# Kernel optimization log

Hardware: AMD Instinct MI355X
Metric: run time of the kernel (lower is better)

Reference implementation:

```python
import jax, jax.numpy as jnp
import numpy as np

N, C, SI, VI, H, R = 10000, 2, 128, 16, 4, 32
SH, VH = SI // H, VI // H  # 32, 4
EPS = 1e-8

def _vnorm(x, axis):
    # clamped L2 norm, matches _norm_no_nan
    return jnp.sqrt(jnp.clip(jnp.sum(x * x, axis=axis), EPS, None))

def _gvp_full(s, v, wh, ws_w, ws_b, wv, wsv_w, wsv_b):
    # GVP with activations=(silu, sigmoid), vector_gate=True, vi=vo
    vh = jnp.swapaxes(v, -1, -2) @ wh            # [..., 3, h]
    vn = _vnorm(vh, -2)                          # [..., h]
    so = jnp.concatenate([s, vn], -1) @ ws_w + ws_b
    vo = jnp.swapaxes(vh @ wv, -1, -2)           # [..., vo, 3]
    gate = jax.nn.sigmoid(jax.nn.sigmoid(so) @ wsv_w + wsv_b)
    return jax.nn.silu(so), vo * gate[..., None]

def setup_inputs():
    key = jax.random.key(0)
    ks = iter(jax.random.split(key, 40))
    def lin(i, o):
        return jax.random.normal(next(ks), (i, o), jnp.float32) / np.sqrt(i)
    def bias(o):
        return 0.02 * jax.random.normal(next(ks), (o,), jnp.float32)
    inp = {}
    inp['s'] = jax.random.normal(next(ks), (N, C, SI), jnp.float32)
    inp['v'] = jax.random.normal(next(ks), (N, C, VI, 3), jnp.float32)
    # weight_proj: GVP((SI,VI)->(R,0)), no activations; h_dim = max(VI,0) = VI
    inp['wp_wh'] = lin(VI, VI); inp['wp_ws_w'] = lin(VI + SI, R); inp['wp_ws_b'] = bias(R)
    # to_q/k/v: GVP((SI,VI)->(SI,VI)), silu/sigmoid, vector_gate; h_dim = VI
    for p in ('q', 'k', 'vv'):
        inp[p + '_wh'] = lin(VI, VI)
        inp[p + '_ws_w'] = lin(VI + SI, SI); inp[p + '_ws_b'] = bias(SI)
        inp[p + '_wv'] = lin(VI, VI)
        inp[p + '_wsv_w'] = lin(SI, VI); inp[p + '_wsv_b'] = bias(VI)
    # attn_gvp_long: GVP((2*SH, 2*VH) -> (1,0)), no activations; h_dim = 2*VH
    inp['attn_wh'] = lin(2 * VH, 2 * VH)
    inp['attn_ws_w'] = lin(2 * VH + 2 * SH, 1); inp['attn_ws_b'] = bias(1)
    return inp

def reference(s, v, wp_wh, wp_ws_w, wp_ws_b,
              q_wh, q_ws_w, q_ws_b, q_wv, q_wsv_w, q_wsv_b,
              k_wh, k_ws_w, k_ws_b, k_wv, k_wsv_w, k_wsv_b,
              vv_wh, vv_ws_w, vv_ws_b, vv_wv, vv_wsv_w, vv_wsv_b,
              attn_wh, attn_ws_w, attn_ws_b):
    n, c = s.shape[:2]
    # ---- Compress: softmax-pool N -> R anchors ----
    vh = jnp.swapaxes(v, -1, -2) @ wp_wh          # [N,C,3,VI]
    vn = _vnorm(vh, -2)                            # [N,C,VI]
    pw = jnp.concatenate([s, vn], -1) @ wp_ws_w + wp_ws_b  # [N,C,R]
    pw = jax.nn.softmax(pw, axis=0)                # softmax over nodes
    s_g = jnp.einsum('nca,ncs->acs', pw, s)        # [R,C,SI] (includes transpose(0,1))
    v_g = jnp.einsum('nca,ncvd->acvd', pw, v)      # [R,C,VI,3]
    # ---- q from nodes, k/v from anchors ----
    qs, qv = _gvp_full(s, v, q_wh, q_ws_w, q_ws_b, q_wv, q_wsv_w, q_wsv_b)
    ks, kv = _gvp_full(s_g, v_g, k_wh, k_ws_w, k_ws_b, k_wv, k_wsv_w, k_wsv_b)
    vs, vv_ = _gvp_full(s_g, v_g, vv_wh, vv_ws_w, vv_ws_b, vv_wv, vv_wsv_w, vv_wsv_b)
    qs = qs.reshape(n, c, H, SH); qv = qv.reshape(n, c, H, VH, 3)
    ks = ks.reshape(R, c, H, SH); kv = kv.reshape(R, c, H, VH, 3)
    vs = vs.reshape(R, c, H, SH); vv_ = vv_.reshape(R, c, H, VH, 3)
    # ---- attention GVP on cat(q, k): split weights instead of materializing concat ----
    wh_q, wh_k = attn_wh[:VH], attn_wh[VH:]        # wh @ cat(qv,kv) = qv@wh_q + kv@wh_k
    qh = jnp.swapaxes(qv, -1, -2) @ wh_q           # [N,C,H,3,2VH]
    kh = jnp.swapaxes(kv, -1, -2) @ wh_k           # [R,C,H,3,2VH]
    vn2 = _vnorm(qh[:, None] + kh[None], -2)       # [N,R,C,H,2VH]
    ws_q = attn_ws_w[:SH]; ws_k = attn_ws_w[SH:2 * SH]; ws_n = attn_ws_w[2 * SH:]
    e = (qs @ ws_q)[:, None] + (ks @ ws_k)[None] + vn2 @ ws_n + attn_ws_b  # [N,R,C,H,1]
    e = e[..., 0] / np.sqrt(SH)
    alpha = jax.nn.softmax(e, axis=1)              # softmax over anchors (dim=1)
    # ---- Broadcast: weighted sum of anchor values ----
    out_s = jnp.einsum('nrch,rchd->nchd', alpha, vs).reshape(n, c, SI)
    out_v = jnp.einsum('nrch,rchde->nchde', alpha, vv_).reshape(n, c, VI, 3)
    return out_s, out_v
```

## Files before the change

kernel.cpp:

```cpp
#include <hip/hip_runtime.h>
#include <hip/hip_bf16.h>


#define N_  10000
#define C_  2
#define SI_ 128
#define VI_ 16
#define H_  4
#define R_  32
#define SH_ 32
#define VH_ 4
#define NC_ (N_*C_)

typedef const float* __restrict__ fptr;

__device__ __forceinline__ float sigm(float x){ return 1.f/(1.f+__expf(-x)); }

#define OFF_LG  0
#define OFF_EQH 640000
#define OFF_SG  2720000
#define OFF_ST  2731264
#define OFF_TKH 2731392
#define OFF_TEK 2737536
#define OFF_TVS 2737792
#define OFF_TVV 2745984

__global__ __launch_bounds__(256) void kA(
    fptr s, fptr v,
    fptr wp_wh, fptr wp_ws_w, fptr wp_ws_b,
    fptr q_wh, fptr q_ws_w, fptr q_ws_b, fptr q_wv, fptr q_wsv_w, fptr q_wsv_b,
    fptr attn_wh, fptr attn_ws_w,
    float* __restrict__ lg, float* __restrict__ eqh)
{
  __shared__ __align__(16) float XT[160*20];
  __shared__ __align__(16) float VVs[16*48];
  __shared__ __align__(16) float VHQ[16*48];
  __shared__ __align__(16) float SO[16*128];
  __shared__ __align__(16) float GATE[16*16];
  __shared__ __align__(16) float QV[16*48];

  const int tid  = threadIdx.x;
  const int row0 = blockIdx.x * 16;

  for (int idx = tid; idx < 16*128; idx += 256){
    int r = idx >> 7, j = idx & 127;
    XT[j*20 + r] = s[(row0+r)*128 + j];
  }
  for (int idx = tid; idx < 16*48; idx += 256){
    int r = idx / 48, k = idx - r*48;
    VVs[r*48 + k] = v[(row0+r)*48 + k];
  }
  __syncthreads();

  for (int t = tid; t < 512; t += 256){
    int r = t >> 5, ii = t & 31, path = ii >> 4, i = ii & 15;
    fptr wh = path ? wp_wh : q_wh;
    float h0=0.f, h1=0.f, h2=0.f;
    #pragma unroll
    for (int j = 0; j < 16; j++){
      float w = wh[j*16 + i];
      h0 = fmaf(VVs[r*48 + j*3 + 0], w, h0);
      h1 = fmaf(VVs[r*48 + j*3 + 1], w, h1);
      h2 = fmaf(VVs[r*48 + j*3 + 2], w, h2);
    }
    float vn = sqrtf(fmaxf(h0*h0 + h1*h1 + h2*h2, 1e-8f));
    if (!path){
      VHQ[r*48 +  0 + i] = h0;
      VHQ[r*48 + 16 + i] = h1;
      VHQ[r*48 + 32 + i] = h2;
      XT[(128+i)*20 + r] = vn;
    } else {
      XT[(144+i)*20 + r] = vn;
    }
  }
  __syncthreads();

  {
    const int col = tid & 127, rg = tid >> 7;
    float bqs = q_ws_b[col];
    float acc[8];
    #pragma unroll
    for (int k = 0; k < 8; k++) acc[k] = bqs;
    #pragma unroll 4
    for (int j = 0; j < 144; j++){
      float w = q_ws_w[j*128 + col];
      const float* xp = &XT[j*20 + rg*8];
      float4 x0 = *(const float4*)xp;
      float4 x1 = *(const float4*)(xp + 4);
      acc[0] = fmaf(x0.x, w, acc[0]); acc[1] = fmaf(x0.y, w, acc[1]);
      acc[2] = fmaf(x0.z, w, acc[2]); acc[3] = fmaf(x0.w, w, acc[3]);
      acc[4] = fmaf(x1.x, w, acc[4]); acc[5] = fmaf(x1.y, w, acc[5]);
      acc[6] = fmaf(x1.z, w, acc[6]); acc[7] = fmaf(x1.w, w, acc[7]);
    }
    #pragma unroll
    for (int k = 0; k < 8; k++) SO[(rg*8 + k)*128 + col] = acc[k];
  }
  {
    const int col = tid & 31, rg = tid >> 5;
    float bp = wp_ws_b[col];
    float a0 = bp, a1 = bp;
    #pragma unroll 4
    for (int j = 0; j < 144; j++){
      int jj = (j < 128) ? j : (j + 16);
      float w = wp_ws_w[j*32 + col];
      const float* xp = &XT[jj*20 + rg*2];
      a0 = fmaf(xp[0], w, a0);
      a1 = fmaf(xp[1], w, a1);
    }
    lg[(row0 + rg*2 + 0)*32 + col] = a0;
    lg[(row0 + rg*2 + 1)*32 + col] = a1;
  }
  __syncthreads();

  {
    const int r = tid >> 4, g = tid & 15;
    float ga = q_wsv_b[g];
    for (int o = 0; o < 128; o++)
      ga = fmaf(sigm(SO[r*128 + o]), q_wsv_w[o*16 + g], ga);
    GATE[r*16 + g] = sigm(ga);
  }
  if (tid < 64){
    const int r = tid >> 2, h = tid & 3;
    float e = 0.f;
    #pragma unroll
    for (int t = 0; t < 32; t++){
      float so = SO[r*128 + h*32 + t];
      e = fmaf(so * sigm(so), attn_ws_w[t], e);
    }
    eqh[(row0 + r)*104 + h] = e;
  }
  __syncthreads();

  for (int t = tid; t < 16*48; t += 256){
    int r = t / 48, k = t - r*48, i = k / 3, d = k - i*3;
    float acc = 0.f;
    #pragma unroll
    for (int j = 0; j < 16; j++)
      acc = fmaf(VHQ[r*48 + d*16 + j], q_wv[j*16 + i], acc);
    QV[r*48 + k] = acc * GATE[r*16 + i];
  }
  __syncthreads();

  for (int t = tid; t < 16*96; t += 256){
    int r = t / 96, k = t - r*96;
    int h = k / 24, rem = k - h*24, d = rem >> 3, ee = rem & 7;
    float acc = 0.f;
    #pragma unroll
    for (int i = 0; i < 4; i++)
      acc = fmaf(QV[r*48 + (h*4 + i)*3 + d], attn_wh[i*8 + ee], acc);
    eqh[(row0 + r)*104 + 8 + k] = acc;
  }
}

__global__ __launch_bounds__(256) void kStats(const float* __restrict__ lg,
                                              float* __restrict__ st)
{
  const int q = blockIdx.x;
  const int c = q >> 5, a = q & 31;
  const int tid = threadIdx.x;
  __shared__ float red[256];

  float m = -1e30f;
  for (int n = tid; n < N_; n += 256)
    m = fmaxf(m, lg[(n*2 + c)*32 + a]);
  red[tid] = m; __syncthreads();
  for (int s2 = 128; s2 > 0; s2 >>= 1){
    if (tid < s2) red[tid] = fmaxf(red[tid], red[tid + s2]);
    __syncthreads();
  }
  const float mx = red[0];
  __syncthreads();

  float sm = 0.f;
  for (int n = tid; n < N_; n += 256)
    sm += __expf(lg[(n*2 + c)*32 + a] - mx);
  red[tid] = sm; __syncthreads();
  for (int s2 = 128; s2 > 0; s2 >>= 1){
    if (tid < s2) red[tid] += red[tid + s2];
    __syncthreads();
  }
  if (tid == 0){ st[q*2] = mx; st[q*2 + 1] = red[0]; }
}

#define CHUNK_ 50
__global__ __launch_bounds__(256) void kAccum(const float* __restrict__ lg,
                                              const float* __restrict__ st,
                                              fptr s, fptr v,
                                              float* __restrict__ sg)
{
  const int b = blockIdx.x, c = b & 1, chunk = b >> 1;
  const int n0 = chunk * CHUNK_;
  const int tid = threadIdx.x;
  const int ag = tid >> 5, dl = tid & 31;

  float mx[4], dn[4];
  #pragma unroll
  for (int aa = 0; aa < 4; aa++){
    int a = ag*4 + aa;
    mx[aa] = st[(c*32 + a)*2];
    dn[aa] = 1.f / st[(c*32 + a)*2 + 1];
  }
  float acc[4][6] = {};
  for (int n = n0; n < n0 + CHUNK_; n++){
    const int rc = n*2 + c;
    float pw[4];
    #pragma unroll
    for (int aa = 0; aa < 4; aa++)
      pw[aa] = __expf(lg[rc*32 + ag*4 + aa] - mx[aa]) * dn[aa];
    #pragma unroll
    for (int dd = 0; dd < 6; dd++){
      int d = dl + 32*dd;
      if (d < 176){
        float xv = (d < 128) ? s[rc*128 + d] : v[rc*48 + d - 128];
        #pragma unroll
        for (int aa = 0; aa < 4; aa++)
          acc[aa][dd] = fmaf(pw[aa], xv, acc[aa][dd]);
      }
    }
  }
  #pragma unroll
  for (int aa = 0; aa < 4; aa++)
    #pragma unroll
    for (int dd = 0; dd < 6; dd++){
      int d = dl + 32*dd;
      if (d < 176)
        atomicAdd(&sg[(c*32 + ag*4 + aa)*176 + d], acc[aa][dd]);
    }
}

__global__ __launch_bounds__(256) void kSmall(
    const float* __restrict__ sg,
    fptr k_wh, fptr k_ws_w, fptr k_ws_b, fptr k_wv, fptr k_wsv_w, fptr k_wsv_b,
    fptr vv_wh, fptr vv_ws_w, fptr vv_ws_b, fptr vv_wv, fptr vv_wsv_w, fptr vv_wsv_b,
    fptr attn_wh, fptr attn_ws_w,
    float* __restrict__ tkh, float* __restrict__ tek,
    float* __restrict__ tvs, float* __restrict__ tvv)
{
  const int b = blockIdx.x, r = b >> 1, c = b & 1;
  const int tid = threadIdx.x;
  __shared__ float X[176];
  __shared__ float VN[2][16];
  __shared__ float VH[2][48];
  __shared__ float SOk[128], SOv[128];
  __shared__ float G[2][16];
  __shared__ float KV[48];

  if (tid < 176) X[tid] = sg[(c*32 + r)*176 + tid];
  __syncthreads();

  if (tid < 32){
    int path = tid >> 4, i = tid & 15;
    fptr wh = path ? vv_wh : k_wh;
    float h0=0.f, h1=0.f, h2=0.f;
    #pragma unroll
    for (int j = 0; j < 16; j++){
      float w = wh[j*16 + i];
      h0 = fmaf(X[128 + j*3 + 0], w, h0);
      h1 = fmaf(X[128 + j*3 + 1], w, h1);
      h2 = fmaf(X[128 + j*3 + 2], w, h2);
    }
    VH[path][ 0 + i] = h0; VH[path][16 + i] = h1; VH[path][32 + i] = h2;
    VN[path][i] = sqrtf(fmaxf(h0*h0 + h1*h1 + h2*h2, 1e-8f));
  }
  __syncthreads();

  {
    int path = tid >> 7, col = tid & 127;
    fptr W  = path ? vv_ws_w : k_ws_w;
    fptr Bb = path ? vv_ws_b : k_ws_b;
    float so = Bb[col];
    for (int j = 0; j < 128; j++) so = fmaf(X[j], W[j*128 + col], so);
    #pragma unroll
    for (int i = 0; i < 16; i++)  so = fmaf(VN[path][i], W[(128+i)*128 + col], so);
    (path ? SOv : SOk)[col] = so;
  }
  __syncthreads();

  if (tid < 32){
    int path = tid >> 4, g = tid & 15;
    fptr Wsv = path ? vv_wsv_w : k_wsv_w;
    fptr Bsv = path ? vv_wsv_b : k_wsv_b;
    const float* SOp = path ? SOv : SOk;
    float ga = Bsv[g];
    for (int o = 0; o < 128; o++)
      ga = fmaf(sigm(SOp[o]), Wsv[o*16 + g], ga);
    G[path][g] = sigm(ga);
  } else if (tid < 36){
    int h = tid - 32;
    float e = 0.f;
    #pragma unroll
    for (int t = 0; t < 32; t++){
      float so = SOk[h*32 + t];
      e = fmaf(so * sigm(so), attn_ws_w[32 + t], e);
    }
    tek[(r*2 + c)*4 + h] = e;
  } else if (tid >= 64 && tid < 192){
    int o = tid - 64;
    float so = SOv[o];
    tvs[(r*2 + c)*128 + o] = so * sigm(so);
  }
  __syncthreads();

  if (tid < 96){
    int path = tid / 48, k = tid % 48, i = k / 3, d = k - i*3;
    fptr Wv = path ? vv_wv : k_wv;
    float vo = 0.f;
    #pragma unroll
    for (int j = 0; j < 16; j++)
      vo = fmaf(VH[path][d*16 + j], Wv[j*16 + i], vo);
    float gv = vo * G[path][i];
    if (path == 0) KV[k] = gv;
    else {
      int h = i >> 2, ii = i & 3;
      tvv[(((r*2 + c)*4 + h)*4 + ii)*3 + d] = gv;
    }
  }
  __syncthreads();

  if (tid < 96){
    int h = tid / 24, rem = tid % 24, d = rem >> 3, ee = rem & 7;
    float acc = 0.f;
    #pragma unroll
    for (int i = 0; i < 4; i++)
      acc = fmaf(KV[(h*4 + i)*3 + d], attn_wh[(4 + i)*8 + ee], acc);
    tkh[((r*2 + c)*4 + h)*24 + d*8 + ee] = acc;
  }
}

__global__ __launch_bounds__(256, 2) void kAttn(
    const float* __restrict__ eqh,
    const float* __restrict__ tkh, const float* __restrict__ tek,
    const float* __restrict__ tvs, const float* __restrict__ tvv,
    fptr attn_ws_w, fptr attn_ws_b,
    float* __restrict__ out)
{
  __shared__ __align__(16) float KH[6144];
  __shared__ __align__(16) float EK[256];
  __shared__ __align__(16) float VS[256*36];
  __shared__ __align__(16) float VVt[3072];
  const int tid = threadIdx.x;

  for (int i = tid; i < 6144; i += 256) KH[i] = tkh[i];
  if (tid < 256) EK[tid] = tek[tid];
  for (int i = tid; i < 8192; i += 256){ int base = i >> 5, t = i & 31; VS[base*36 + t] = tvs[i]; }
  for (int i = tid; i < 3072; i += 256) VVt[i] = tvv[i];

  float wsn[8];
  #pragma unroll
  for (int ee = 0; ee < 8; ee++) wsn[ee] = attn_ws_w[64 + ee];
  const float wb = attn_ws_b[0];
  __syncthreads();

  const int row = blockIdx.x*64 + (tid >> 2);
  const int h = tid & 3;
  if (row < NC_){
    const int c = row & 1;
    const float eq = eqh[row*104 + h];
    float qh[24];
    const float4* qp = (const float4*)&eqh[row*104 + 8 + h*24];
    #pragma unroll
    for (int k = 0; k < 6; k++){
      float4 t4 = qp[k];
      qh[k*4+0] = t4.x; qh[k*4+1] = t4.y; qh[k*4+2] = t4.z; qh[k*4+3] = t4.w;
    }
    float e[32];
    float em = -1e30f;
    #pragma unroll
    for (int r = 0; r < 32; r++){
      const int base = (r*2 + c)*4 + h;
      const float* khp = &KH[base*24];
      float en = 0.f;
      #pragma unroll
      for (int ee = 0; ee < 8; ee++){
        float a0 = qh[ee]      + khp[ee];
        float a1 = qh[8 + ee]  + khp[8 + ee];
        float a2 = qh[16 + ee] + khp[16 + ee];
        en = fmaf(sqrtf(fmaxf(a0*a0 + a1*a1 + a2*a2, 1e-8f)), wsn[ee], en);
      }
      float ev = (eq + EK[base] + en + wb) * 0.17677669529663687f;
      e[r] = ev; em = fmaxf(em, ev);
    }
    float den = 0.f;
    #pragma unroll
    for (int r = 0; r < 32; r++){ e[r] = __expf(e[r] - em); den += e[r]; }
    const float inv = 1.f / den;
    float accs[32] = {};
    float accv[12] = {};
    #pragma unroll
    for (int r = 0; r < 32; r++){
      const int base = (r*2 + c)*4 + h;
      const float al = e[r] * inv;
      const float* vsp = &VS[base*36];
      #pragma unroll
      for (int t = 0; t < 32; t++) accs[t] = fmaf(al, vsp[t], accs[t]);
      const float* vvp = &VVt[base*12];
      #pragma unroll
      for (int k = 0; k < 12; k++) accv[k] = fmaf(al, vvp[k], accv[k]);
    }
    float* po = &out[row*128 + h*32];
    #pragma unroll
    for (int t = 0; t < 32; t++) po[t] = accs[t];
    float* pv = &out[NC_*128 + row*48 + h*12];
    #pragma unroll
    for (int k = 0; k < 12; k++) pv[k] = accv[k];
  }
}

extern "C" void kernel_launch(void* const* d_in, const int* in_sizes, int n_in,
                              void* d_out, int out_size, void* d_ws, size_t ws_size,
                              hipStream_t stream)
{
  fptr s        = (fptr)d_in[0];
  fptr v        = (fptr)d_in[1];
  fptr wp_wh    = (fptr)d_in[2];
  fptr wp_ws_w  = (fptr)d_in[3];
  fptr wp_ws_b  = (fptr)d_in[4];
  fptr q_wh     = (fptr)d_in[5];
  fptr q_ws_w   = (fptr)d_in[6];
  fptr q_ws_b   = (fptr)d_in[7];
  fptr q_wv     = (fptr)d_in[8];
  fptr q_wsv_w  = (fptr)d_in[9];
  fptr q_wsv_b  = (fptr)d_in[10];
  fptr k_wh     = (fptr)d_in[11];
  fptr k_ws_w   = (fptr)d_in[12];
  fptr k_ws_b   = (fptr)d_in[13];
  fptr k_wv     = (fptr)d_in[14];
  fptr k_wsv_w  = (fptr)d_in[15];
  fptr k_wsv_b  = (fptr)d_in[16];
  fptr vv_wh    = (fptr)d_in[17];
  fptr vv_ws_w  = (fptr)d_in[18];
  fptr vv_ws_b  = (fptr)d_in[19];
  fptr vv_wv    = (fptr)d_in[20];
  fptr vv_wsv_w = (fptr)d_in[21];
  fptr vv_wsv_b = (fptr)d_in[22];
  fptr attn_wh  = (fptr)d_in[23];
  fptr attn_ws_w= (fptr)d_in[24];
  fptr attn_ws_b= (fptr)d_in[25];

  float* ws  = (float*)d_ws;
  float* lg  = ws + OFF_LG;
  float* eqh = ws + OFF_EQH;
  float* sg  = ws + OFF_SG;
  float* st  = ws + OFF_ST;
  float* tkh = ws + OFF_TKH;
  float* tek = ws + OFF_TEK;
  float* tvs = ws + OFF_TVS;
  float* tvv = ws + OFF_TVV;

  hipMemsetAsync(sg, 0, 11264*sizeof(float), stream);

  kA<<<NC_/16, 256, 0, stream>>>(s, v, wp_wh, wp_ws_w, wp_ws_b,
                                 q_wh, q_ws_w, q_ws_b, q_wv, q_wsv_w, q_wsv_b,
                                 attn_wh, attn_ws_w, lg, eqh);
  kStats<<<64, 256, 0, stream>>>(lg, st);
  kAccum<<<2*(N_/CHUNK_), 256, 0, stream>>>(lg, st, s, v, sg);
  kSmall<<<64, 256, 0, stream>>>(sg,
                                 k_wh, k_ws_w, k_ws_b, k_wv, k_wsv_w, k_wsv_b,
                                 vv_wh, vv_ws_w, vv_ws_b, vv_wv, vv_wsv_w, vv_wsv_b,
                                 attn_wh, attn_ws_w, tkh, tek, tvs, tvv);
  kAttn<<<(NC_ + 63)/64, 256, 0, stream>>>(eqh, tkh, tek, tvs, tvv,
                                           attn_ws_w, attn_ws_b, (float*)d_out);
}
```

Measured before the change: 272.0 us.

## Transpose logits layout, precompute sigmoid once, and widen attention blocks

```diff
diff --git a/kernel.cpp b/kernel.cpp
--- a/kernel.cpp
+++ b/kernel.cpp
@@ -32,12 +32,14 @@
     fptr attn_wh, fptr attn_ws_w,
     float* __restrict__ lg, float* __restrict__ eqh)
 {
-  __shared__ __align__(16) float XT[160*20];
+  __shared__ __align__(16) float ARENA[160*20];
   __shared__ __align__(16) float VVs[16*48];
   __shared__ __align__(16) float VHQ[16*48];
   __shared__ __align__(16) float SO[16*128];
   __shared__ __align__(16) float GATE[16*16];
   __shared__ __align__(16) float QV[16*48];
+  float* const XT  = ARENA;
+  float* const SIG = ARENA;
 
   const int tid  = threadIdx.x;
   const int row0 = blockIdx.x * 16;
@@ -75,16 +77,16 @@
   }
   __syncthreads();
 
+  const int colA = tid & 127, rgA = tid >> 7;
+  float acc[8];
   {
-    const int col = tid & 127, rg = tid >> 7;
-    float bqs = q_ws_b[col];
-    float acc[8];
+    float bqs = q_ws_b[colA];
     #pragma unroll
     for (int k = 0; k < 8; k++) acc[k] = bqs;
     #pragma unroll 4
     for (int j = 0; j < 144; j++){
-      float w = q_ws_w[j*128 + col];
-      const float* xp = &XT[j*20 + rg*8];
+      float w = q_ws_w[j*128 + colA];
+      const float* xp = &XT[j*20 + rgA*8];
       float4 x0 = *(const float4*)xp;
       float4 x1 = *(const float4*)(xp + 4);
       acc[0] = fmaf(x0.x, w, acc[0]); acc[1] = fmaf(x0.y, w, acc[1]);
@@ -92,8 +94,6 @@
       acc[4] = fmaf(x1.x, w, acc[4]); acc[5] = fmaf(x1.y, w, acc[5]);
       acc[6] = fmaf(x1.z, w, acc[6]); acc[7] = fmaf(x1.w, w, acc[7]);
     }
-    #pragma unroll
-    for (int k = 0; k < 8; k++) SO[(rg*8 + k)*128 + col] = acc[k];
   }
   {
     const int col = tid & 31, rg = tid >> 5;
@@ -107,48 +107,62 @@
       a0 = fmaf(xp[0], w, a0);
       a1 = fmaf(xp[1], w, a1);
     }
-    lg[(row0 + rg*2 + 0)*32 + col] = a0;
-    lg[(row0 + rg*2 + 1)*32 + col] = a1;
+    const int n = (row0 >> 1) + rg;
+    lg[(     col)*N_ + n] = a0;
+    lg[(32 + col)*N_ + n] = a1;
+  }
+  __syncthreads();
+
+  #pragma unroll
+  for (int k = 0; k < 8; k++){
+    float so = acc[k];
+    float sg_ = sigm(so);
+    SIG[(rgA*8 + k)*128 + colA] = sg_;
+    SO [(rgA*8 + k)*128 + colA] = so * sg_;
   }
   __syncthreads();
 
   {
     const int r = tid >> 4, g = tid & 15;
     float ga = q_wsv_b[g];
-    for (int o = 0; o < 128; o++)
-      ga = fmaf(sigm(SO[r*128 + o]), q_wsv_w[o*16 + g], ga);
+    #pragma unroll 8
+    for (int o = 0; o < 128; o += 4){
+      float4 s4 = *(const float4*)&SIG[r*128 + o];
+      ga = fmaf(s4.x, q_wsv_w[(o+0)*16 + g], ga);
+      ga = fmaf(s4.y, q_wsv_w[(o+1)*16 + g], ga);
+      ga = fmaf(s4.z, q_wsv_w[(o+2)*16 + g], ga);
+      ga = fmaf(s4.w, q_wsv_w[(o+3)*16 + g], ga);
+    }
     GATE[r*16 + g] = sigm(ga);
   }
   if (tid < 64){
     const int r = tid >> 2, h = tid & 3;
     float e = 0.f;
     #pragma unroll
-    for (int t = 0; t < 32; t++){
-      float so = SO[r*128 + h*32 + t];
-      e = fmaf(so * sigm(so), attn_ws_w[t], e);
-    }
+    for (int t = 0; t < 32; t++)
+      e = fmaf(SO[r*128 + h*32 + t], attn_ws_w[t], e);
     eqh[(row0 + r)*104 + h] = e;
   }
   __syncthreads();
 
   for (int t = tid; t < 16*48; t += 256){
     int r = t / 48, k = t - r*48, i = k / 3, d = k - i*3;
-    float acc = 0.f;
+    float a = 0.f;
     #pragma unroll
     for (int j = 0; j < 16; j++)
-      acc = fmaf(VHQ[r*48 + d*16 + j], q_wv[j*16 + i], acc);
-    QV[r*48 + k] = acc * GATE[r*16 + i];
+      a = fmaf(VHQ[r*48 + d*16 + j], q_wv[j*16 + i], a);
+    QV[r*48 + k] = a * GATE[r*16 + i];
   }
   __syncthreads();
 
   for (int t = tid; t < 16*96; t += 256){
     int r = t / 96, k = t - r*96;
     int h = k / 24, rem = k - h*24, d = rem >> 3, ee = rem & 7;
-    float acc = 0.f;
+    float a = 0.f;
     #pragma unroll
     for (int i = 0; i < 4; i++)
-      acc = fmaf(QV[r*48 + (h*4 + i)*3 + d], attn_wh[i*8 + ee], acc);
-    eqh[(row0 + r)*104 + 8 + k] = acc;
+      a = fmaf(QV[r*48 + (h*4 + i)*3 + d], attn_wh[i*8 + ee], a);
+    eqh[(row0 + r)*104 + 8 + k] = a;
   }
 }
 
@@ -156,13 +170,12 @@
                                               float* __restrict__ st)
 {
   const int q = blockIdx.x;
-  const int c = q >> 5, a = q & 31;
   const int tid = threadIdx.x;
+  const float* col = lg + q*N_;
   __shared__ float red[256];
 
   float m = -1e30f;
-  for (int n = tid; n < N_; n += 256)
-    m = fmaxf(m, lg[(n*2 + c)*32 + a]);
+  for (int n = tid; n < N_; n += 256) m = fmaxf(m, col[n]);
   red[tid] = m; __syncthreads();
   for (int s2 = 128; s2 > 0; s2 >>= 1){
     if (tid < s2) red[tid] = fmaxf(red[tid], red[tid + s2]);
@@ -172,8 +185,7 @@
   __syncthreads();
 
   float sm = 0.f;
-  for (int n = tid; n < N_; n += 256)
-    sm += __expf(lg[(n*2 + c)*32 + a] - mx);
+  for (int n = tid; n < N_; n += 256) sm += __expf(col[n] - mx);
   red[tid] = sm; __syncthreads();
   for (int s2 = 128; s2 > 0; s2 >>= 1){
     if (tid < s2) red[tid] += red[tid + s2];
@@ -206,7 +218,7 @@
     float pw[4];
     #pragma unroll
     for (int aa = 0; aa < 4; aa++)
-      pw[aa] = __expf(lg[rc*32 + ag*4 + aa] - mx[aa]) * dn[aa];
+      pw[aa] = __expf(lg[(c*32 + ag*4 + aa)*N_ + n] - mx[aa]) * dn[aa];
     #pragma unroll
     for (int dd = 0; dd < 6; dd++){
       int d = dl + 32*dd;
@@ -319,15 +331,15 @@
 
   if (tid < 96){
     int h = tid / 24, rem = tid % 24, d = rem >> 3, ee = rem & 7;
-    float acc = 0.f;
+    float a = 0.f;
     #pragma unroll
     for (int i = 0; i < 4; i++)
-      acc = fmaf(KV[(h*4 + i)*3 + d], attn_wh[(4 + i)*8 + ee], acc);
-    tkh[((r*2 + c)*4 + h)*24 + d*8 + ee] = acc;
-  }
-}
-
-__global__ __launch_bounds__(256, 2) void kAttn(
+      a = fmaf(KV[(h*4 + i)*3 + d], attn_wh[(4 + i)*8 + ee], a);
+    tkh[((r*2 + c)*4 + h)*24 + d*8 + ee] = a;
+  }
+}
+
+__global__ __launch_bounds__(512) void kAttn(
     const float* __restrict__ eqh,
     const float* __restrict__ tkh, const float* __restrict__ tek,
     const float* __restrict__ tvs, const float* __restrict__ tvv,
@@ -340,10 +352,10 @@
   __shared__ __align__(16) float VVt[3072];
   const int tid = threadIdx.x;
 
-  for (int i = tid; i < 6144; i += 256) KH[i] = tkh[i];
+  for (int i = tid; i < 6144; i += 512) KH[i] = tkh[i];
   if (tid < 256) EK[tid] = tek[tid];
-  for (int i = tid; i < 8192; i += 256){ int base = i >> 5, t = i & 31; VS[base*36 + t] = tvs[i]; }
-  for (int i = tid; i < 3072; i += 256) VVt[i] = tvv[i];
+  for (int i = tid; i < 8192; i += 512){ int base = i >> 5, t = i & 31; VS[base*36 + t] = tvs[i]; }
+  for (int i = tid; i < 3072; i += 512) VVt[i] = tvv[i];
 
   float wsn[8];
   #pragma unroll
@@ -351,7 +363,7 @@
   const float wb = attn_ws_b[0];
   __syncthreads();
 
-  const int row = blockIdx.x*64 + (tid >> 2);
+  const int row = blockIdx.x*128 + (tid >> 2);
   const int h = tid & 3;
   if (row < NC_){
     const int c = row & 1;
@@ -458,6 +470,6 @@
                                  k_wh, k_ws_w, k_ws_b, k_wv, k_wsv_w, k_wsv_b,
                                  vv_wh, vv_ws_w, vv_ws_b, vv_wv, vv_wsv_w, vv_wsv_b,
                                  attn_wh, attn_ws_w, tkh, tek, tvs, tvv);
-  kAttn<<<(NC_ + 63)/64, 256, 0, stream>>>(eqh, tkh, tek, tvs, tvv,
-                                           attn_ws_w, attn_ws_b, (float*)d_out);
-}
+  kAttn<<<(NC_ + 127)/128, 512, 0, stream>>>(eqh, tkh, tek, tvs, tvv,
+                                             attn_ws_w, attn_ws_b, (float*)d_out);
+}
```

New measurement: 253.2 us. 6.9% less time.
